# Kernel optimization log

Measured on AMD Instinct MI355X. Metric: run time of the kernel, lower is better.

The kernel has to match this reference:

```python
import jax, jax.numpy as jnp
import numpy as np

LATENT, U_DIM, NUM_PROD, NUM_INJ, FEAT_C = 128, 30, 20, 10, 128
WELL_IN = LATENT + U_DIM + FEAT_C  # 286
HID = 64
B = 16384


def setup_inputs() -> dict:
    key = jax.random.key(0)
    ks = jax.random.split(key, 12)
    s = lambda fan_in: 1.0 / np.sqrt(fan_in)
    return {
        "zt": jax.random.normal(ks[0], (B, LATENT), jnp.float32),
        "dt": 1,
        "ut": jax.random.normal(ks[1], (B, U_DIM), jnp.float32),
        "well_features": jax.random.normal(ks[2], (B, NUM_PROD, FEAT_C), jnp.float32),
        # StructuredODEFunc params: dz/dt = -(L L^T) z + Bm u
        "L": jax.random.normal(ks[3], (LATENT, LATENT), jnp.float32) * s(LATENT),
        "Bm": jax.random.normal(ks[4], (LATENT, U_DIM), jnp.float32) * s(U_DIM),
        # per-well MLP heads, stacked: [P, in, out]
        "W1": jax.random.uniform(ks[5], (NUM_PROD, WELL_IN, HID), jnp.float32, -s(WELL_IN), s(WELL_IN)),
        "b1": jax.random.uniform(ks[6], (NUM_PROD, HID), jnp.float32, -s(WELL_IN), s(WELL_IN)),
        "W2": jax.random.uniform(ks[7], (NUM_PROD, HID, 2), jnp.float32, -s(HID), s(HID)),
        "b2": jax.random.uniform(ks[8], (NUM_PROD, 2), jnp.float32, -s(HID), s(HID)),
        # injector head: Linear(latent+u_dim, num_inj)
        "Wi": jax.random.uniform(ks[9], (LATENT + U_DIM, NUM_INJ), jnp.float32, -s(LATENT + U_DIM), s(LATENT + U_DIM)),
        "bi": jax.random.uniform(ks[10], (NUM_INJ,), jnp.float32, -s(LATENT + U_DIM), s(LATENT + U_DIM)),
    }


def reference(zt, dt, ut, well_features, L, Bm, W1, b1, W2, b2, Wi, bi):
    # ODE step: A = -L L^T, f(z) = A z + Bm u; euler over t_span [0,1] -> one step h=1
    A = -(L @ L.T)                                  # [D, D]
    zt1 = zt + zt @ A.T + ut @ Bm.T                 # [B, D]
    zu = jnp.concatenate([zt1, ut], axis=-1)        # [B, D+U]
    # per-well heads, fused as batched gather-MLP
    zu_b = jnp.broadcast_to(zu[:, None, :], (zu.shape[0], NUM_PROD, zu.shape[1]))
    head_in = jnp.concatenate([zu_b, well_features], axis=-1)        # [B, P, WELL_IN]
    h = jax.nn.relu(jnp.einsum('bpi,pih->bph', head_in, W1) + b1)    # [B, P, 64]
    well_out = jnp.einsum('bph,pho->bpo', h, W2) + b2                # [B, P, 2]
    well_out = well_out.reshape(well_out.shape[0], NUM_PROD * 2)     # concat order matches loop
    inj_out = zu @ Wi + bi                                           # [B, num_inj]
    yt1 = jnp.concatenate([well_out, inj_out], axis=-1)              # [B, 2P+I]
    return zt1, yt1
```

## Files before the change

kernel.cpp:

```cpp
#include <hip/hip_runtime.h>

#define BATCH   16384
#define LATENT  128
#define U_DIM   30
#define NUM_PROD 20
#define NUM_INJ 10
#define FEAT_C  128
#define WELL_IN 286
#define HID     64
#define ZT1_N   (BATCH*LATENT)
#define OUT_ROW (NUM_PROD*2+NUM_INJ)

typedef unsigned short u16;
typedef __attribute__((ext_vector_type(8))) short  short8;
typedef __attribute__((ext_vector_type(4))) float  floatx4;

__device__ __forceinline__ u16 f2bf(float f){
    unsigned x = __builtin_bit_cast(unsigned, f);
    x += 0x7fffu + ((x >> 16) & 1u);
    return (u16)(x >> 16);
}
__device__ __forceinline__ short8 cvt8(floatx4 a, floatx4 b){
    short8 s;
    s[0]=(short)f2bf(a[0]); s[1]=(short)f2bf(a[1]);
    s[2]=(short)f2bf(a[2]); s[3]=(short)f2bf(a[3]);
    s[4]=(short)f2bf(b[0]); s[5]=(short)f2bf(b[1]);
    s[6]=(short)f2bf(b[2]); s[7]=(short)f2bf(b[3]);
    return s;
}

#define NW1  368640
#define NGS  20480
#define NWIS 2560
#define NW2S 20480
__device__ u16 g_w1s[NW1];
__device__ u16 g_gs [NGS];
__device__ u16 g_wis[NWIS];
__device__ u16 g_w2s[NW2S];

__global__ __launch_bounds__(256) void prep_kernel(
    const float* __restrict__ L, const float* __restrict__ Bm,
    const float* __restrict__ W1, const float* __restrict__ Wi,
    const float* __restrict__ W2)
{
    const int bx = blockIdx.x, t = threadIdx.x;
    if (bx < 180) {
        int s = bx*256 + t;
        int lane = s & 63;
        int rest = s >> 6;
        int kk = rest % 9, pn = rest / 9;
        int n0 = pn & 3, p = pn >> 2;
        int kbase = kk*32 + ((lane>>4)*8);
        int n = n0*16 + (lane & 15);
        short8 v;
#pragma unroll
        for (int j = 0; j < 8; j++) {
            int k = kbase + j;
            u16 b = 0;
            if (k < 158)        b = f2bf(W1[(p*WELL_IN + k)*HID + n]);
            else if (k >= 160)  b = f2bf(W1[(p*WELL_IN + (k-2))*HID + n]);
            v[j] = (short)b;
        }
        *(short8*)&g_w1s[(size_t)s*8] = v;
        return;
    }
    if (bx < 272) {
        int sid = (bx-180)*256 + t;
        if (sid < NW2S) {
            int j=sid&7, lane=(sid>>3)&63, rest=sid>>9;
            int kk=rest&1, p=rest>>1;
            int k=kk*32+((lane>>4)*8)+j, n=lane&15;
            g_w2s[sid] = (n<2) ? f2bf(W2[(p*HID+k)*2+n]) : (u16)0;
            return;
        }
        sid -= NW2S;
        if (sid < NWIS) {
            int j=sid&7, lane=(sid>>3)&63, kk=sid>>9;
            int k=kk*32+((lane>>4)*8)+j, n=lane&15;
            g_wis[sid] = (k<158 && n<NUM_INJ) ? f2bf(Wi[k*NUM_INJ+n]) : (u16)0;
            return;
        }
        sid -= NWIS;
        if (sid < 512) {
            int lane=sid&63, nt=sid>>6;
            int q=lane>>4, n=nt*16+(lane&15);
#pragma unroll
            for (int j = 0; j < 8; j++) {
                int u = q*8 + j;
                float v = (u < U_DIM) ? Bm[n*U_DIM + u] : 0.f;
                g_gs[((nt*5+4)*64 + lane)*8 + j] = f2bf(v);
            }
        }
        return;
    }
    const int mt = bx - 272;
    const int w = t>>6, lane=t&63, q=lane>>4, m=lane&15;
    floatx4 accG[2];
    accG[0]=(floatx4){0.f,0.f,0.f,0.f}; accG[1]=(floatx4){0.f,0.f,0.f,0.f};
#pragma unroll
    for (int kk = 0; kk < 4; kk++) {
        const float* ap = &L[(mt*16+m)*128 + kk*32 + q*8];
        short8 a = cvt8(*(const floatx4*)ap, *(const floatx4*)(ap+4));
#pragma unroll
        for (int ntl = 0; ntl < 2; ntl++) {
            int nt = w*2 + ntl;
            const float* bp = &L[(nt*16+m)*128 + kk*32 + q*8];
            short8 b = cvt8(*(const floatx4*)bp, *(const floatx4*)(bp+4));
            accG[ntl] = __builtin_amdgcn_mfma_f32_16x16x32_bf16(a, b, accG[ntl], 0, 0, 0);
        }
    }
#pragma unroll
    for (int ntl = 0; ntl < 2; ntl++)
#pragma unroll
        for (int r = 0; r < 4; r++) {
            int kg = mt*16 + q*4 + r;
            int n  = (w*2+ntl)*16 + m;
            float v = ((kg==n) ? 1.f : 0.f) - accG[ntl][r];
            int fi = ((n>>4)*5 + (kg>>5))*512 + (((kg>>3)&3)*16 + (n&15))*8 + (kg&7);
            g_gs[fi] = f2bf(v);
        }
}

__global__ __launch_bounds__(512) void ker_main(
    const float* __restrict__ zt, const float* __restrict__ ut,
    const float* __restrict__ wff, const float* __restrict__ b1,
    const float* __restrict__ b2,  const float* __restrict__ bi,
    const float* __restrict__ W2g,
    float* __restrict__ outf)
{
    __shared__ alignas(16) u16   zus[32][168];
    __shared__ alignas(16) u16   wfb0[4096];
    __shared__ alignas(16) u16   wfb1[4096];
    __shared__ alignas(16) float outs[32][50];
    __shared__ alignas(16) float w2l[2560];
    __shared__ alignas(16) float b1l[1280];
    const int t = threadIdx.x;
    const int row0 = blockIdx.x * 32;
    const int w = t >> 6, lane = t & 63, q = lane >> 4, m = lane & 15;
    const int n0 = w & 3, rt = w >> 2;

    const int lane_s = t & 63, cs = (t >> 6) & 3, rts = t >> 8;
    const int qs = lane_s >> 4, ms = lane_s & 15;

    floatx4 rA[2], rB[2];
    auto issue = [&](floatx4 (&r)[2], int p){
        const float* pb = &wff[((size_t)(row0 + rts*16 + ms)*NUM_PROD + p)*FEAT_C + cs*32 + qs*8];
        r[0] = *(const floatx4*)pb;
        r[1] = *(const floatx4*)(pb + 4);
    };
    auto cstore = [&](const floatx4 (&r)[2], u16* __restrict__ wfb){
        *(short8*)&wfb[((rts*4 + cs)*64 + lane_s)*8] = cvt8(r[0], r[1]);
    };

    issue(rA, 0);
    issue(rB, 1);

    for (int i = t; i < 1024; i += 512) {
        int r = i >> 5, c4 = i & 31;
        floatx4 v = *(const floatx4*)&zt[(size_t)(row0 + r)*128 + c4*4];
        u16* d = &zus[r][c4*4];
        d[0]=f2bf(v[0]); d[1]=f2bf(v[1]); d[2]=f2bf(v[2]); d[3]=f2bf(v[3]);
    }
    for (int i = t; i < 32*U_DIM; i += 512) {
        int r = i / U_DIM, c = i - r*U_DIM;
        zus[r][128 + c] = f2bf(ut[(row0 + r)*U_DIM + c]);
    }
    if (t < 64) zus[t >> 1][158 + (t & 1)] = 0;
    for (int i = t; i < 2560; i += 512) w2l[i] = W2g[i];
    for (int i = t; i < 1280; i += 512) b1l[i] = b1[i];
    for (int i = t; i < 1600; i += 512) {
        int col = i % 50;
        (&outs[0][0])[i] = (col < 40) ? b2[col] : 0.f;
    }
    __syncthreads();

    {
        const int mt = w & 1, ng = (w >> 1) * 2;
        floatx4 acc[2];
        acc[0] = (floatx4){0.f,0.f,0.f,0.f};
        acc[1] = (floatx4){0.f,0.f,0.f,0.f};
#pragma unroll
        for (int kk = 0; kk < 5; kk++) {
            short8 a = *(const short8*)&zus[mt*16 + m][kk*32 + q*8];
#pragma unroll
            for (int c = 0; c < 2; c++) {
                short8 b = *(const short8*)&g_gs[(((ng+c)*5 + kk)*64 + lane)*8];
                acc[c] = __builtin_amdgcn_mfma_f32_16x16x32_bf16(a, b, acc[c], 0, 0, 0);
            }
        }
        __syncthreads();
#pragma unroll
        for (int c = 0; c < 2; c++)
#pragma unroll
            for (int r = 0; r < 4; r++) {
                int row = mt*16 + q*4 + r;
                int col = (ng+c)*16 + m;
                float v = acc[c][r];
                outf[(size_t)(row0 + row)*128 + col] = v;
                zus[row][col] = f2bf(v);
            }
    }
    __syncthreads();

    short8 za[5];
#pragma unroll
    for (int kk = 0; kk < 5; kk++)
        za[kk] = *(const short8*)&zus[rt*16 + m][kk*32 + q*8];

    if (n0 == 3) {
        floatx4 ai = (floatx4){0.f,0.f,0.f,0.f};
#pragma unroll
        for (int kk = 0; kk < 5; kk++) {
            short8 b = *(const short8*)&g_wis[(kk*64 + lane)*8];
            ai = __builtin_amdgcn_mfma_f32_16x16x32_bf16(za[kk], b, ai, 0, 0, 0);
        }
        if (m < NUM_INJ) {
            float bv = bi[m];
#pragma unroll
            for (int r = 0; r < 4; r++)
                outs[rt*16 + q*4 + r][40 + m] = ai[r] + bv;
        }
    }

    short8 bfrA[9], bfrB[9];
    auto loadB = [&](short8 (&bfr)[9], int p){
#pragma unroll
        for (int kk = 0; kk < 9; kk++)
            bfr[kk] = *(const short8*)&g_w1s[(((size_t)p*36 + n0*9 + kk)*64 + lane)*8];
    };
    loadB(bfrA, 0);

    auto do_well = [&](int p, const u16* __restrict__ wfb,
                       const short8 (&bfrC)[9], short8 (&bfrN)[9]){
        if (p < 19) loadB(bfrN, p + 1);
        floatx4 acc = (floatx4){0.f,0.f,0.f,0.f};
#pragma unroll
        for (int kk = 0; kk < 9; kk++) {
            short8 a = (kk < 5) ? za[kk]
                     : *(const short8*)&wfb[((rt*4 + kk-5)*64 + lane)*8];
            acc = __builtin_amdgcn_mfma_f32_16x16x32_bf16(a, bfrC[kk], acc, 0, 0, 0);
        }
        const int col = n0*16 + m;
        const float bb = b1l[p*64 + col];
        const float w2x = w2l[(p*64 + col)*2 + 0];
        const float w2y = w2l[(p*64 + col)*2 + 1];
        float s[8];
#pragma unroll
        for (int r = 0; r < 4; r++) {
            float h = acc[r] + bb;
            h = h > 0.f ? h : 0.f;
            s[r*2+0] = h * w2x;
            s[r*2+1] = h * w2y;
        }
#pragma unroll
        for (int mask = 1; mask < 16; mask <<= 1)
#pragma unroll
            for (int i = 0; i < 8; i++)
                s[i] += __shfl_xor(s[i], mask);
        float val = (m==0)?s[0]:(m==1)?s[1]:(m==2)?s[2]:(m==3)?s[3]
                   :(m==4)?s[4]:(m==5)?s[5]:(m==6)?s[6]:s[7];
        if (m < 8)
            atomicAdd(&outs[rt*16 + q*4 + (m>>1)][p*2 + (m&1)], val);
    };

    for (int tb = 0; tb < 20; tb += 2) {
        cstore(rA, wfb0);
        __syncthreads();
        if (tb + 2 < 20) issue(rA, tb + 2);
        do_well(tb, wfb0, bfrA, bfrB);
        cstore(rB, wfb1);
        __syncthreads();
        if (tb + 3 < 20) issue(rB, tb + 3);
        do_well(tb + 1, wfb1, bfrB, bfrA);
    }
    __syncthreads();

    {
        const float* of = &outs[0][0];
        float* dst = outf + (size_t)ZT1_N + (size_t)row0 * OUT_ROW;
        for (int i = t; i < 400; i += 512)
            *(floatx4*)&dst[i*4] = *(const floatx4*)&of[i*4];
    }
}

extern "C" void kernel_launch(void* const* d_in, const int* in_sizes, int n_in,
                              void* d_out, int out_size, void* d_ws, size_t ws_size,
                              hipStream_t stream)
{
    const float* zt = (const float*)d_in[0];
    const float* ut = (const float*)d_in[2];
    const float* wf = (const float*)d_in[3];
    const float* L  = (const float*)d_in[4];
    const float* Bm = (const float*)d_in[5];
    const float* W1 = (const float*)d_in[6];
    const float* b1 = (const float*)d_in[7];
    const float* W2 = (const float*)d_in[8];
    const float* b2 = (const float*)d_in[9];
    const float* Wi = (const float*)d_in[10];
    const float* bi = (const float*)d_in[11];
    float* outf = (float*)d_out;

    prep_kernel<<<280, 256, 0, stream>>>(L, Bm, W1, Wi, W2);
    ker_main<<<512, 512, 0, stream>>>(zt, ut, wf, b1, b2, bi, W2, outf);
}
```

Measured before the change: 322.4 us.

## Assign whole wells per wave with 16-row blocks and register-resident features

Reworks the main kernel so each 256-thread block handles 16 rows and each wave owns entire wells, computing all 64 hidden units itself instead of splitting hidden columns across waves. Well features are loaded directly into registers and double-buffered per wave, which removes the shared-memory staging, the per-well block barriers and the shared atomics. Biases and W2 are now read from global memory inside the loop instead of being staged in shared memory. The cost is more registers per wave and W1 fragments being loaded without prefetch. Smaller blocks with a launch-bounds hint of 4 blocks per CU aim for higher occupancy.

Measured after the change: 299.1 us. 7.2% less time.

```diff
diff --git a/kernel.cpp b/kernel.cpp
--- a/kernel.cpp
+++ b/kernel.cpp
@@ -121,67 +121,51 @@
         }
 }
 
-__global__ __launch_bounds__(512) void ker_main(
+__global__ __launch_bounds__(256, 4) void ker_main(
     const float* __restrict__ zt, const float* __restrict__ ut,
     const float* __restrict__ wff, const float* __restrict__ b1,
     const float* __restrict__ b2,  const float* __restrict__ bi,
     const float* __restrict__ W2g,
     float* __restrict__ outf)
 {
-    __shared__ alignas(16) u16   zus[32][168];
-    __shared__ alignas(16) u16   wfb0[4096];
-    __shared__ alignas(16) u16   wfb1[4096];
-    __shared__ alignas(16) float outs[32][50];
-    __shared__ alignas(16) float w2l[2560];
-    __shared__ alignas(16) float b1l[1280];
+    __shared__ alignas(16) u16   zus[16][168];
+    __shared__ alignas(16) float outs[16][50];
     const int t = threadIdx.x;
-    const int row0 = blockIdx.x * 32;
+    const int row0 = blockIdx.x * 16;
     const int w = t >> 6, lane = t & 63, q = lane >> 4, m = lane & 15;
-    const int n0 = w & 3, rt = w >> 2;
-
-    const int lane_s = t & 63, cs = (t >> 6) & 3, rts = t >> 8;
-    const int qs = lane_s >> 4, ms = lane_s & 15;
-
-    floatx4 rA[2], rB[2];
-    auto issue = [&](floatx4 (&r)[2], int p){
-        const float* pb = &wff[((size_t)(row0 + rts*16 + ms)*NUM_PROD + p)*FEAT_C + cs*32 + qs*8];
-        r[0] = *(const floatx4*)pb;
-        r[1] = *(const floatx4*)(pb + 4);
+
+    floatx4 fA[8], fB[8];
+    auto issue = [&](floatx4 (&f)[8], int p){
+#pragma unroll
+        for (int kk = 0; kk < 4; kk++) {
+            const float* pb = &wff[((size_t)(row0 + m)*NUM_PROD + p)*FEAT_C + kk*32 + q*8];
+            f[kk*2+0] = *(const floatx4*)pb;
+            f[kk*2+1] = *(const floatx4*)(pb + 4);
+        }
     };
-    auto cstore = [&](const floatx4 (&r)[2], u16* __restrict__ wfb){
-        *(short8*)&wfb[((rts*4 + cs)*64 + lane_s)*8] = cvt8(r[0], r[1]);
-    };
-
-    issue(rA, 0);
-    issue(rB, 1);
-
-    for (int i = t; i < 1024; i += 512) {
+    issue(fA, w);
+
+    for (int i = t; i < 512; i += 256) {
         int r = i >> 5, c4 = i & 31;
         floatx4 v = *(const floatx4*)&zt[(size_t)(row0 + r)*128 + c4*4];
         u16* d = &zus[r][c4*4];
         d[0]=f2bf(v[0]); d[1]=f2bf(v[1]); d[2]=f2bf(v[2]); d[3]=f2bf(v[3]);
     }
-    for (int i = t; i < 32*U_DIM; i += 512) {
+    for (int i = t; i < 480; i += 256) {
         int r = i / U_DIM, c = i - r*U_DIM;
         zus[r][128 + c] = f2bf(ut[(row0 + r)*U_DIM + c]);
     }
-    if (t < 64) zus[t >> 1][158 + (t & 1)] = 0;
-    for (int i = t; i < 2560; i += 512) w2l[i] = W2g[i];
-    for (int i = t; i < 1280; i += 512) b1l[i] = b1[i];
-    for (int i = t; i < 1600; i += 512) {
-        int col = i % 50;
-        (&outs[0][0])[i] = (col < 40) ? b2[col] : 0.f;
-    }
+    if (t < 32) zus[t >> 1][158 + (t & 1)] = 0;
     __syncthreads();
 
     {
-        const int mt = w & 1, ng = (w >> 1) * 2;
+        const int ng = w * 2;
         floatx4 acc[2];
         acc[0] = (floatx4){0.f,0.f,0.f,0.f};
         acc[1] = (floatx4){0.f,0.f,0.f,0.f};
 #pragma unroll
         for (int kk = 0; kk < 5; kk++) {
-            short8 a = *(const short8*)&zus[mt*16 + m][kk*32 + q*8];
+            short8 a = *(const short8*)&zus[m][kk*32 + q*8];
 #pragma unroll
             for (int c = 0; c < 2; c++) {
                 short8 b = *(const short8*)&g_gs[(((ng+c)*5 + kk)*64 + lane)*8];
@@ -193,7 +177,7 @@
         for (int c = 0; c < 2; c++)
 #pragma unroll
             for (int r = 0; r < 4; r++) {
-                int row = mt*16 + q*4 + r;
+                int row = q*4 + r;
                 int col = (ng+c)*16 + m;
                 float v = acc[c][r];
                 outf[(size_t)(row0 + row)*128 + col] = v;
@@ -202,55 +186,62 @@
     }
     __syncthreads();
 
-    short8 za[5];
-#pragma unroll
-    for (int kk = 0; kk < 5; kk++)
-        za[kk] = *(const short8*)&zus[rt*16 + m][kk*32 + q*8];
-
-    if (n0 == 3) {
+    issue(fB, w + 4);
+
+    if (w == 3) {
         floatx4 ai = (floatx4){0.f,0.f,0.f,0.f};
 #pragma unroll
         for (int kk = 0; kk < 5; kk++) {
+            short8 a = *(const short8*)&zus[m][kk*32 + q*8];
             short8 b = *(const short8*)&g_wis[(kk*64 + lane)*8];
-            ai = __builtin_amdgcn_mfma_f32_16x16x32_bf16(za[kk], b, ai, 0, 0, 0);
+            ai = __builtin_amdgcn_mfma_f32_16x16x32_bf16(a, b, ai, 0, 0, 0);
         }
         if (m < NUM_INJ) {
             float bv = bi[m];
 #pragma unroll
             for (int r = 0; r < 4; r++)
-                outs[rt*16 + q*4 + r][40 + m] = ai[r] + bv;
-        }
-    }
-
-    short8 bfrA[9], bfrB[9];
-    auto loadB = [&](short8 (&bfr)[9], int p){
-#pragma unroll
-        for (int kk = 0; kk < 9; kk++)
-            bfr[kk] = *(const short8*)&g_w1s[(((size_t)p*36 + n0*9 + kk)*64 + lane)*8];
-    };
-    loadB(bfrA, 0);
-
-    auto do_well = [&](int p, const u16* __restrict__ wfb,
-                       const short8 (&bfrC)[9], short8 (&bfrN)[9]){
-        if (p < 19) loadB(bfrN, p + 1);
-        floatx4 acc = (floatx4){0.f,0.f,0.f,0.f};
+                outs[q*4 + r][40 + m] = ai[r] + bv;
+        }
+    }
+
+    auto proc = [&](int p, const floatx4 (&f)[8]){
+        short8 wa[4];
+#pragma unroll
+        for (int kk = 0; kk < 4; kk++) wa[kk] = cvt8(f[kk*2+0], f[kk*2+1]);
+        float bb[4], w2x[4], w2y[4];
+#pragma unroll
+        for (int n0 = 0; n0 < 4; n0++) {
+            int col = n0*16 + m;
+            bb[n0]  = b1[p*64 + col];
+            w2x[n0] = W2g[(p*64 + col)*2 + 0];
+            w2y[n0] = W2g[(p*64 + col)*2 + 1];
+        }
+        float bb2 = b2[p*2 + (m & 1)];
+        floatx4 hacc[4];
+#pragma unroll
+        for (int n0 = 0; n0 < 4; n0++) hacc[n0] = (floatx4){0.f,0.f,0.f,0.f};
 #pragma unroll
         for (int kk = 0; kk < 9; kk++) {
-            short8 a = (kk < 5) ? za[kk]
-                     : *(const short8*)&wfb[((rt*4 + kk-5)*64 + lane)*8];
-            acc = __builtin_amdgcn_mfma_f32_16x16x32_bf16(a, bfrC[kk], acc, 0, 0, 0);
-        }
-        const int col = n0*16 + m;
-        const float bb = b1l[p*64 + col];
-        const float w2x = w2l[(p*64 + col)*2 + 0];
-        const float w2y = w2l[(p*64 + col)*2 + 1];
+            short8 a = (kk < 5) ? *(const short8*)&zus[m][kk*32 + q*8]
+                                : wa[kk-5];
+#pragma unroll
+            for (int n0 = 0; n0 < 4; n0++) {
+                short8 b = *(const short8*)&g_w1s[(((size_t)p*36 + n0*9 + kk)*64 + lane)*8];
+                hacc[n0] = __builtin_amdgcn_mfma_f32_16x16x32_bf16(a, b, hacc[n0], 0, 0, 0);
+            }
+        }
         float s[8];
 #pragma unroll
         for (int r = 0; r < 4; r++) {
-            float h = acc[r] + bb;
-            h = h > 0.f ? h : 0.f;
-            s[r*2+0] = h * w2x;
-            s[r*2+1] = h * w2y;
+            float s0 = 0.f, s1 = 0.f;
+#pragma unroll
+            for (int n0 = 0; n0 < 4; n0++) {
+                float h = hacc[n0][r] + bb[n0];
+                h = h > 0.f ? h : 0.f;
+                s0 += h * w2x[n0];
+                s1 += h * w2y[n0];
+            }
+            s[r*2+0] = s0; s[r*2+1] = s1;
         }
 #pragma unroll
         for (int mask = 1; mask < 16; mask <<= 1)
@@ -260,25 +251,20 @@
         float val = (m==0)?s[0]:(m==1)?s[1]:(m==2)?s[2]:(m==3)?s[3]
                    :(m==4)?s[4]:(m==5)?s[5]:(m==6)?s[6]:s[7];
         if (m < 8)
-            atomicAdd(&outs[rt*16 + q*4 + (m>>1)][p*2 + (m&1)], val);
+            outs[q*4 + (m>>1)][p*2 + (m&1)] = val + bb2;
     };
 
-    for (int tb = 0; tb < 20; tb += 2) {
-        cstore(rA, wfb0);
-        __syncthreads();
-        if (tb + 2 < 20) issue(rA, tb + 2);
-        do_well(tb, wfb0, bfrA, bfrB);
-        cstore(rB, wfb1);
-        __syncthreads();
-        if (tb + 3 < 20) issue(rB, tb + 3);
-        do_well(tb + 1, wfb1, bfrB, bfrA);
-    }
+    proc(w,      fA);  issue(fA, w + 8);
+    proc(w + 4,  fB);  issue(fB, w + 12);
+    proc(w + 8,  fA);  issue(fA, w + 16);
+    proc(w + 12, fB);
+    proc(w + 16, fA);
     __syncthreads();
 
     {
         const float* of = &outs[0][0];
         float* dst = outf + (size_t)ZT1_N + (size_t)row0 * OUT_ROW;
-        for (int i = t; i < 400; i += 512)
+        for (int i = t; i < 200; i += 256)
             *(floatx4*)&dst[i*4] = *(const floatx4*)&of[i*4];
     }
 }
@@ -301,5 +287,5 @@
     float* outf = (float*)d_out;
 
     prep_kernel<<<280, 256, 0, stream>>>(L, Bm, W1, Wi, W2);
-    ker_main<<<512, 512, 0, stream>>>(zt, ut, wf, b1, b2, bi, W2, outf);
-}
+    ker_main<<<BATCH/16, 256, 0, stream>>>(zt, ut, wf, b1, b2, bi, W2, outf);
+}
```
